# Kernel optimization log

Measured on AMD Instinct MI355X. Metric: run time of the kernel, lower is better.

## Reference

```python
import jax, jax.numpy as jnp
import numpy as np

N, NFEAT, NHID, NCLASS = 8192, 128, 128, 40


def _init(key, shape, fan_in):
    return jax.random.normal(key, shape, jnp.float32) / np.sqrt(fan_in).astype(np.float32)


def setup_inputs() -> dict:
    ks = jax.random.split(jax.random.key(0), 8)
    return {
        "x": jax.random.normal(ks[0], (N, NFEAT), jnp.float32),
        # dense normalized adjacency: row-stochastic-ish positive matrix
        "adj": jax.random.uniform(ks[1], (N, N), jnp.float32) * (2.0 / N),
        "W_emb": _init(ks[2], (NFEAT, NHID), NFEAT),
        "b_emb": jnp.zeros((NHID,), jnp.float32),
        "W_gc1": _init(ks[3], (NHID, NHID), NHID),
        "b_gc1": jnp.zeros((NHID,), jnp.float32),
        "W_e": _init(ks[4], (2 * NHID, NHID), 2 * NHID),
        "b_e": jnp.zeros((NHID,), jnp.float32),
        "W_gc2": _init(ks[5], (NHID, NCLASS), NHID),
        "b_gc2": jnp.zeros((NCLASS,), jnp.float32),
        "fully_connected_graph": 1,  # unused by forward (passed but never read)
    }


def reference(x, adj, W_emb, b_emb, W_gc1, b_gc1, W_e, b_e, W_gc2, b_gc2,
              fully_connected_graph):
    nhid = W_emb.shape[1]
    # x = self.emb(x)
    h = x @ W_emb + b_emb  # [N, nhid]

    # Edge branch. Original materializes edge_feat[i*N+j] = concat(h[i], h[j])
    # ([N*N, 2*nhid]) then GraphConvolution_edge: support = edge_feat @ W_e,
    # reshaped [N, N, nhid], aggregated x_e[i] = sum_j adj[i,j] * support[i,j] + b_e.
    # Algebraically identical fused form (same math, no O(N^2*nhid) tensor):
    #   support[i,j] = h[i] @ W_e[:nhid] + h[j] @ W_e[nhid:]
    #   x_e[i] = deg[i] * (h[i] @ W_e_src) + (adj @ (h @ W_e_dst))[i] + b_e
    s_src = h @ W_e[:nhid]   # [N, nhid]
    s_dst = h @ W_e[nhid:]   # [N, nhid]
    deg = adj.sum(axis=1, keepdims=True)  # [N, 1] row sums
    x_e = deg * s_src + adj @ s_dst + b_e  # [N, nhid]

    # Node branch: gc1 -> relu -> dropout(eval: identity) -> gc2 -> log_softmax
    h1 = jax.nn.relu(adj @ (h @ W_gc1) + b_gc1)       # [N, nhid]
    logits = adj @ (h1 @ W_gc2) + b_gc2               # [N, nclass]
    out = jax.nn.log_softmax(logits, axis=1)
    return out, x_e
```

## Files before the change

### kernel.cpp

```cpp
#include <hip/hip_runtime.h>

#define DI __device__ __forceinline__

using f32x4  = __attribute__((ext_vector_type(4))) float;
using bf16x8 = __attribute__((ext_vector_type(8))) __bf16;
using u16x4  = __attribute__((ext_vector_type(4))) unsigned short;
using u32x4  = __attribute__((ext_vector_type(4))) unsigned int;

constexpr int NNODE = 8192;

DI unsigned short f2bf(float f) {
    unsigned int u = __builtin_bit_cast(unsigned int, f);
    u += 0x7fffu + ((u >> 16) & 1u);
    return (unsigned short)(u >> 16);
}
DI float bf2f(unsigned short s) {
    return __builtin_bit_cast(float, (unsigned int)s << 16);
}

DI int swz256(int r, int cb) { return r * 256 + (cb ^ ((r & 15) << 4)); }
DI int swz128(int r, int cb) { return r * 128 + (cb ^ ((r & 7) << 4)); }

__global__ void prep_w(const float* __restrict__ W_emb, const float* __restrict__ W_e,
                       const float* __restrict__ W_gc1, const float* __restrict__ W_gc2,
                       unsigned short* __restrict__ WembT_hi, unsigned short* __restrict__ WembT_lo,
                       unsigned short* __restrict__ WcatT_hi, unsigned short* __restrict__ WcatT_lo,
                       unsigned short* __restrict__ Wg2T_hi, unsigned short* __restrict__ Wg2T_lo)
{
    int gid = blockIdx.x * 256 + threadIdx.x;
    if (gid >= 576 * 128) return;
    int k = gid & 127, n = gid >> 7;
    float v;
    unsigned short *dh, *dl;
    if (n < 128) {
        v = W_emb[k * 128 + n];
        dh = WembT_hi + n * 128 + k; dl = WembT_lo + n * 128 + k;
    } else if (n < 512) {
        int m = n - 128;
        if (m < 128)      v = W_e[k * 128 + m];
        else if (m < 256) v = W_e[(k + 128) * 128 + (m - 128)];
        else              v = W_gc1[k * 128 + (m - 256)];
        dh = WcatT_hi + m * 128 + k; dl = WcatT_lo + m * 128 + k;
    } else {
        int c = n - 512;
        v = (c < 40) ? W_gc2[k * 40 + c] : 0.f;
        dh = Wg2T_hi + c * 128 + k; dl = Wg2T_lo + c * 128 + k;
    }
    unsigned short hi = f2bf(v);
    *dh = hi;
    *dl = f2bf(v - bf2f(hi));
}

template<int NCHUNK, int AKIND, int OUTKIND>
__global__ __launch_bounds__(256) void small_gemm(
    const float* __restrict__ Af32,
    const unsigned short* __restrict__ A_hi, const unsigned short* __restrict__ A_lo,
    const unsigned short* __restrict__ Bt_hi, const unsigned short* __restrict__ Bt_lo,
    const float* __restrict__ bias,
    unsigned short* __restrict__ out_hi, unsigned short* __restrict__ out_lo,
    float* __restrict__ out_s,
    unsigned short* __restrict__ out_t)
{
    __shared__ unsigned short Ah[64 * 128], Al[64 * 128];
    __shared__ unsigned short Bh[NCHUNK * 128], Bl[NCHUNK * 128];
    char* Ahc = (char*)Ah; char* Alc = (char*)Al;
    char* Bhc = (char*)Bh; char* Blc = (char*)Bl;

    const int tid = threadIdx.x;
    const int r0 = blockIdx.x * 64;
    const int n0 = blockIdx.y * NCHUNK;

    if constexpr (AKIND == 0) {
        #pragma unroll
        for (int p = 0; p < 8; ++p) {
            int idx = tid + 256 * p, r = idx >> 5, c4 = idx & 31;
            f32x4 v = *(const f32x4*)(Af32 + (size_t)(r0 + r) * 128 + c4 * 4);
            u16x4 ph, pl;
            #pragma unroll
            for (int j = 0; j < 4; ++j) {
                unsigned short hi = f2bf(v[j]);
                ph[j] = hi; pl[j] = f2bf(v[j] - bf2f(hi));
            }
            *(u16x4*)(Ahc + swz256(r, c4 * 8)) = ph;
            *(u16x4*)(Alc + swz256(r, c4 * 8)) = pl;
        }
    } else {
        #pragma unroll
        for (int p = 0; p < 4; ++p) {
            int idx = tid + 256 * p, r = idx >> 4, c = idx & 15;
            u32x4 vh = *(const u32x4*)(A_hi + (size_t)(r0 + r) * 128 + c * 8);
            u32x4 vl = *(const u32x4*)(A_lo + (size_t)(r0 + r) * 128 + c * 8);
            *(u32x4*)(Ahc + swz256(r, c * 16)) = vh;
            *(u32x4*)(Alc + swz256(r, c * 16)) = vl;
        }
    }
    #pragma unroll
    for (int p = 0; p < NCHUNK / 16; ++p) {
        int idx = tid + 256 * p, r = idx >> 4, c = idx & 15;
        u32x4 vh = *(const u32x4*)(Bt_hi + (size_t)(n0 + r) * 128 + c * 8);
        u32x4 vl = *(const u32x4*)(Bt_lo + (size_t)(n0 + r) * 128 + c * 8);
        *(u32x4*)(Bhc + swz256(r, c * 16)) = vh;
        *(u32x4*)(Blc + swz256(r, c * 16)) = vl;
    }
    __syncthreads();

    const int lane = tid & 63, wid = tid >> 6;
    const int lrow = lane & 15, lkb = (lane >> 4) * 16;
    constexpr int FN = NCHUNK / 16;
    f32x4 acc[FN];
    #pragma unroll
    for (int i = 0; i < FN; ++i) acc[i] = f32x4{0.f, 0.f, 0.f, 0.f};

    const int arow = wid * 16 + lrow;
    #pragma unroll
    for (int kk = 0; kk < 4; ++kk) {
        bf16x8 ah = *(const bf16x8*)(Ahc + swz256(arow, kk * 64 + lkb));
        bf16x8 al = *(const bf16x8*)(Alc + swz256(arow, kk * 64 + lkb));
        #pragma unroll
        for (int nf = 0; nf < FN; ++nf) {
            bf16x8 bh = *(const bf16x8*)(Bhc + swz256(nf * 16 + lrow, kk * 64 + lkb));
            bf16x8 bl = *(const bf16x8*)(Blc + swz256(nf * 16 + lrow, kk * 64 + lkb));
            acc[nf] = __builtin_amdgcn_mfma_f32_16x16x32_bf16(ah, bh, acc[nf], 0, 0, 0);
            acc[nf] = __builtin_amdgcn_mfma_f32_16x16x32_bf16(ah, bl, acc[nf], 0, 0, 0);
            acc[nf] = __builtin_amdgcn_mfma_f32_16x16x32_bf16(al, bh, acc[nf], 0, 0, 0);
        }
    }

    const int rowb = r0 + wid * 16 + ((lane >> 4) << 2);
    #pragma unroll
    for (int nf = 0; nf < FN; ++nf) {
        const int col = n0 + nf * 16 + lrow;
        if constexpr (OUTKIND == 0) {
            float bv = bias[col];
            #pragma unroll
            for (int j = 0; j < 4; ++j) {
                float v = acc[nf][j] + bv;
                unsigned short hi = f2bf(v);
                out_hi[(size_t)(rowb + j) * 128 + col] = hi;
                out_lo[(size_t)(rowb + j) * 128 + col] = f2bf(v - bf2f(hi));
            }
        } else if constexpr (OUTKIND == 1) {
            if (col < 128) {
                #pragma unroll
                for (int j = 0; j < 4; ++j)
                    out_s[(size_t)(rowb + j) * 128 + col] = acc[nf][j];
            } else {
                u16x4 pk = { f2bf(acc[nf][0]), f2bf(acc[nf][1]), f2bf(acc[nf][2]), f2bf(acc[nf][3]) };
                *(u16x4*)(out_t + (size_t)(col - 128) * NNODE + rowb) = pk;
            }
        } else {
            u16x4 pk = { f2bf(acc[nf][0]), f2bf(acc[nf][1]), f2bf(acc[nf][2]), f2bf(acc[nf][3]) };
            *(u16x4*)(out_t + (size_t)col * NNODE + rowb) = pk;
        }
    }
}

template<int NCOLS, int KSPLIT, bool DEG, bool REV>
__global__ __launch_bounds__(512, 4) void adj_gemm(
    const float* __restrict__ adj,
    const unsigned short* __restrict__ Bt,
    float* __restrict__ Tpart,
    float* __restrict__ deg)
{
    __shared__ unsigned short A_lds[2][64 * 64];
    __shared__ unsigned short B_lds[2][NCOLS * 64];

    const int tid = threadIdx.x;
    const int r0 = blockIdx.x * 64;
    const int ks = blockIdx.y;
    constexpr int KLEN = NNODE / KSPLIT;
    constexpr int NT = KLEN / 64;
    const int kbase = ks * KLEN;

    constexpr int NB = NCOLS / 64;
    f32x4 areg[2];
    u32x4 breg[NB];
    float dsum0 = 0.f, dsum1 = 0.f;
    const int ar0 = tid >> 4, ac4 = tid & 15;

    const int lane = tid & 63, wid = tid >> 6;
    constexpr int FM = (NCOLS == 256) ? 2 : 1;
    constexpr int FN = (NCOLS == 256) ? 4 : 2;
    const int wr = (NCOLS == 256) ? (wid >> 2) : (wid >> 1);
    const int wc = (NCOLS == 256) ? (wid & 3) : (wid & 1);
    const int row_w = wr * FM * 16, col_w = wc * FN * 16;
    const int lrow = lane & 15, lkb = (lane >> 4) * 16;

    f32x4 acc[FM][FN];
    #pragma unroll
    for (int fm = 0; fm < FM; ++fm)
        #pragma unroll
        for (int fn = 0; fn < FN; ++fn) acc[fm][fn] = f32x4{0.f, 0.f, 0.f, 0.f};

    auto order = [&](int tt) { return REV ? (NT - 1 - tt) : tt; };

    auto loadG = [&](int t) {
        const int kt = kbase + t * 64;
        #pragma unroll
        for (int p = 0; p < 2; ++p) {
            areg[p] = *(const f32x4*)(adj + (size_t)(r0 + ar0 + 32 * p) * NNODE + kt + ac4 * 4);
            if (DEG) {
                float s = areg[p][0] + areg[p][1] + areg[p][2] + areg[p][3];
                if (p == 0) dsum0 += s; else dsum1 += s;
            }
        }
        #pragma unroll
        for (int p = 0; p < NB; ++p) {
            const int idx = tid + 512 * p, n = idx >> 3, c = idx & 7;
            breg[p] = *(const u32x4*)(Bt + (size_t)n * NNODE + kt + c * 8);
        }
    };
    auto storeL = [&](int buf) {
        char* Ac = (char*)(A_lds[buf]);
        char* Bc = (char*)(B_lds[buf]);
        #pragma unroll
        for (int p = 0; p < 2; ++p) {
            u16x4 pk = { f2bf(areg[p][0]), f2bf(areg[p][1]), f2bf(areg[p][2]), f2bf(areg[p][3]) };
            *(u16x4*)(Ac + swz128(ar0 + 32 * p, ac4 * 8)) = pk;
        }
        #pragma unroll
        for (int p = 0; p < NB; ++p) {
            const int idx = tid + 512 * p, n = idx >> 3, c = idx & 7;
            *(u32x4*)(Bc + swz128(n, c * 16)) = breg[p];
        }
    };

    loadG(order(0));
    storeL(0);
    for (int tt = 0; tt < NT; ++tt) {
        if (tt + 1 < NT) loadG(order(tt + 1));
        __syncthreads();
        const char* Ac = (const char*)(A_lds[tt & 1]);
        const char* Bc = (const char*)(B_lds[tt & 1]);
        #pragma unroll
        for (int kk = 0; kk < 2; ++kk) {
            bf16x8 a[FM], b[FN];
            #pragma unroll
            for (int fm = 0; fm < FM; ++fm)
                a[fm] = *(const bf16x8*)(Ac + swz128(row_w + fm * 16 + lrow, kk * 64 + lkb));
            #pragma unroll
            for (int fn = 0; fn < FN; ++fn)
                b[fn] = *(const bf16x8*)(Bc + swz128(col_w + fn * 16 + lrow, kk * 64 + lkb));
            #pragma unroll
            for (int fm = 0; fm < FM; ++fm)
                #pragma unroll
                for (int fn = 0; fn < FN; ++fn)
                    acc[fm][fn] = __builtin_amdgcn_mfma_f32_16x16x32_bf16(a[fm], b[fn], acc[fm][fn], 0, 0, 0);
        }
        if (tt + 1 < NT) storeL((tt + 1) & 1);
    }

    float* outp = Tpart + (size_t)ks * NNODE * NCOLS;
    #pragma unroll
    for (int fm = 0; fm < FM; ++fm) {
        const int grow0 = r0 + row_w + fm * 16 + ((lane >> 4) << 2);
        #pragma unroll
        for (int fn = 0; fn < FN; ++fn) {
            const int gcol = col_w + fn * 16 + lrow;
            #pragma unroll
            for (int j = 0; j < 4; ++j)
                outp[(size_t)(grow0 + j) * NCOLS + gcol] = acc[fm][fn][j];
        }
    }

    if (DEG) {
        __syncthreads();
        float* sc = (float*)(&A_lds[0][0]);
        sc[tid] = dsum0;
        sc[512 + tid] = dsum1;
        __syncthreads();
        if (tid < 64) {
            const int base = (tid < 32) ? tid * 16 : (512 + (tid - 32) * 16);
            float s = 0.f;
            #pragma unroll
            for (int i = 0; i < 16; ++i) s += sc[base + i];
            atomicAdd(deg + r0 + tid, s);
        }
    }
}

template<int KSPLIT>
__global__ void post1(const float* __restrict__ tA,
                      const float* __restrict__ s_src,
                      const float* __restrict__ deg,
                      const float* __restrict__ b_e,
                      const float* __restrict__ b_gc1,
                      float* __restrict__ x_e_out,
                      unsigned short* __restrict__ h1_hi, unsigned short* __restrict__ h1_lo)
{
    int gid = blockIdx.x * 256 + threadIdx.x;
    int i = gid >> 7, c = gid & 127;
    const size_t o = (size_t)i * 256;
    float t_sdst = 0.f, t_g1 = 0.f;
    #pragma unroll
    for (int p = 0; p < KSPLIT; ++p) {
        const size_t op = (size_t)p * NNODE * 256 + o;
        t_sdst += tA[op + c];
        t_g1   += tA[op + 128 + c];
    }
    x_e_out[gid] = deg[i] * s_src[gid] + t_sdst + b_e[c];
    float h1 = t_g1 + b_gc1[c];
    h1 = h1 > 0.f ? h1 : 0.f;
    unsigned short hi = f2bf(h1);
    h1_hi[gid] = hi;
    h1_lo[gid] = f2bf(h1 - bf2f(hi));
}

template<int KSPLIT>
__global__ void logsm(const float* __restrict__ tB,
                      const float* __restrict__ b_gc2,
                      float* __restrict__ out)
{
    const int wid = threadIdx.x >> 6, lane = threadIdx.x & 63;
    const int row = blockIdx.x * 4 + wid;
    float v = -1e30f;
    if (lane < 40) {
        float s = b_gc2[lane];
        #pragma unroll
        for (int p = 0; p < KSPLIT; ++p)
            s += tB[(size_t)p * NNODE * 64 + (size_t)row * 64 + lane];
        v = s;
    }
    float m = v;
    #pragma unroll
    for (int off = 32; off; off >>= 1) m = fmaxf(m, __shfl_xor(m, off, 64));
    float e = (lane < 40) ? expf(v - m) : 0.f;
    float s = e;
    #pragma unroll
    for (int off = 32; off; off >>= 1) s += __shfl_xor(s, off, 64);
    if (lane < 40) out[(size_t)row * 40 + lane] = v - m - logf(s);
}

extern "C" void kernel_launch(void* const* d_in, const int* in_sizes, int n_in,
                              void* d_out, int out_size, void* d_ws, size_t ws_size,
                              hipStream_t stream)
{
    const float* x     = (const float*)d_in[0];
    const float* adj   = (const float*)d_in[1];
    const float* W_emb = (const float*)d_in[2];
    const float* b_emb = (const float*)d_in[3];
    const float* W_gc1 = (const float*)d_in[4];
    const float* b_gc1 = (const float*)d_in[5];
    const float* W_e   = (const float*)d_in[6];
    const float* b_e   = (const float*)d_in[7];
    const float* W_gc2 = (const float*)d_in[8];
    const float* b_gc2 = (const float*)d_in[9];

    constexpr int KSA = 4;
    constexpr int KSB = 8;

    char* p = (char*)d_ws;
    auto take = [&](size_t bytes) { char* q = p; p += (bytes + 255) & ~(size_t)255; return q; };

    unsigned short* WembT_hi = (unsigned short*)take(128 * 128 * 2);
    unsigned short* WembT_lo = (unsigned short*)take(128 * 128 * 2);
    unsigned short* WcatT_hi = (unsigned short*)take(384 * 128 * 2);
    unsigned short* WcatT_lo = (unsigned short*)take(384 * 128 * 2);
    unsigned short* Wg2T_hi  = (unsigned short*)take(64 * 128 * 2);
    unsigned short* Wg2T_lo  = (unsigned short*)take(64 * 128 * 2);
    unsigned short* h_hi     = (unsigned short*)take((size_t)NNODE * 128 * 2);
    unsigned short* h_lo     = (unsigned short*)take((size_t)NNODE * 128 * 2);
    float*          s_src    = (float*)take((size_t)NNODE * 128 * 4);
    unsigned short* B_A      = (unsigned short*)take((size_t)256 * NNODE * 2);
    float*          tA       = (float*)take((size_t)KSA * NNODE * 256 * 4);
    float*          deg      = (float*)take((size_t)NNODE * 4);
    unsigned short* B_B   = (unsigned short*)s_src;
    float*          tB    = tA;
    unsigned short* h1_hi = h_hi;
    unsigned short* h1_lo = h_lo;

    float* out_ls = (float*)d_out;
    float* x_e    = (float*)d_out + (size_t)NNODE * 40;

    hipMemsetAsync(deg, 0, NNODE * sizeof(float), stream);
    prep_w<<<288, 256, 0, stream>>>(W_emb, W_e, W_gc1, W_gc2,
                                    WembT_hi, WembT_lo, WcatT_hi, WcatT_lo, Wg2T_hi, Wg2T_lo);
    small_gemm<128, 0, 0><<<dim3(128, 1), 256, 0, stream>>>(
        x, nullptr, nullptr, WembT_hi, WembT_lo, b_emb, h_hi, h_lo, nullptr, nullptr);
    small_gemm<128, 1, 1><<<dim3(128, 3), 256, 0, stream>>>(
        nullptr, h_hi, h_lo, WcatT_hi, WcatT_lo, nullptr, nullptr, nullptr, s_src, B_A);
    adj_gemm<256, KSA, true, false><<<dim3(128, KSA), 512, 0, stream>>>(adj, B_A, tA, deg);
    post1<KSA><<<4096, 256, 0, stream>>>(tA, s_src, deg, b_e, b_gc1, x_e, h1_hi, h1_lo);
    small_gemm<64, 1, 2><<<dim3(128, 1), 256, 0, stream>>>(
        nullptr, h1_hi, h1_lo, Wg2T_hi, Wg2T_lo, nullptr, nullptr, nullptr, nullptr, B_B);
    adj_gemm<64, KSB, false, true><<<dim3(128, KSB), 512, 0, stream>>>(adj, B_B, tB, nullptr);
    logsm<KSB><<<2048, 256, 0, stream>>>(tB, b_gc2, out_ls);
}
```

Baseline: 164.5 us.

## Cache bf16 copy of adjacency in first pass and reuse it in second pass

The first adjacency GEMM now writes the bf16-converted adj tiles to a workspace buffer. The second adjacency GEMM reads that half-size bf16 copy instead of the fp32 matrix and skips the conversion. The K-split factors for both GEMMs are halved and the occupancy hint in launch bounds is dropped. This adds a large 128MB write in the first pass and needs extra workspace, so total DRAM traffic is roughly unchanged unless the copy stays in the last-level cache.

```diff
diff --git a/kernel.cpp b/kernel.cpp
--- a/kernel.cpp
+++ b/kernel.cpp
@@ -155,9 +155,11 @@
     }
 }
 
-template<int NCOLS, int KSPLIT, bool DEG, bool REV>
-__global__ __launch_bounds__(512, 4) void adj_gemm(
-    const float* __restrict__ adj,
+template<int NCOLS, int KSPLIT, bool DEG, bool REV, int AMODE>
+__global__ __launch_bounds__(512) void adj_gemm(
+    const float* __restrict__ adjf,
+    const unsigned short* __restrict__ adjb,
+    unsigned short* __restrict__ adjb_out,
     const unsigned short* __restrict__ Bt,
     float* __restrict__ Tpart,
     float* __restrict__ deg)
@@ -174,9 +176,11 @@
 
     constexpr int NB = NCOLS / 64;
     f32x4 areg[2];
+    u32x4 aregb;
     u32x4 breg[NB];
     float dsum0 = 0.f, dsum1 = 0.f;
     const int ar0 = tid >> 4, ac4 = tid & 15;
+    const int br0 = tid >> 3, bc = tid & 7;
 
     const int lane = tid & 63, wid = tid >> 6;
     constexpr int FM = (NCOLS == 256) ? 2 : 1;
@@ -196,13 +200,17 @@
 
     auto loadG = [&](int t) {
         const int kt = kbase + t * 64;
-        #pragma unroll
-        for (int p = 0; p < 2; ++p) {
-            areg[p] = *(const f32x4*)(adj + (size_t)(r0 + ar0 + 32 * p) * NNODE + kt + ac4 * 4);
-            if (DEG) {
-                float s = areg[p][0] + areg[p][1] + areg[p][2] + areg[p][3];
-                if (p == 0) dsum0 += s; else dsum1 += s;
+        if constexpr (AMODE == 0) {
+            #pragma unroll
+            for (int p = 0; p < 2; ++p) {
+                areg[p] = *(const f32x4*)(adjf + (size_t)(r0 + ar0 + 32 * p) * NNODE + kt + ac4 * 4);
+                if (DEG) {
+                    float s = areg[p][0] + areg[p][1] + areg[p][2] + areg[p][3];
+                    if (p == 0) dsum0 += s; else dsum1 += s;
+                }
             }
+        } else {
+            aregb = *(const u32x4*)(adjb + (size_t)(r0 + br0) * NNODE + kt + bc * 8);
         }
         #pragma unroll
         for (int p = 0; p < NB; ++p) {
@@ -210,13 +218,19 @@
             breg[p] = *(const u32x4*)(Bt + (size_t)n * NNODE + kt + c * 8);
         }
     };
-    auto storeL = [&](int buf) {
+    auto storeL = [&](int buf, int t) {
+        const int kt = kbase + t * 64;
         char* Ac = (char*)(A_lds[buf]);
         char* Bc = (char*)(B_lds[buf]);
-        #pragma unroll
-        for (int p = 0; p < 2; ++p) {
-            u16x4 pk = { f2bf(areg[p][0]), f2bf(areg[p][1]), f2bf(areg[p][2]), f2bf(areg[p][3]) };
-            *(u16x4*)(Ac + swz128(ar0 + 32 * p, ac4 * 8)) = pk;
+        if constexpr (AMODE == 0) {
+            #pragma unroll
+            for (int p = 0; p < 2; ++p) {
+                u16x4 pk = { f2bf(areg[p][0]), f2bf(areg[p][1]), f2bf(areg[p][2]), f2bf(areg[p][3]) };
+                *(u16x4*)(Ac + swz128(ar0 + 32 * p, ac4 * 8)) = pk;
+                *(u16x4*)(adjb_out + (size_t)(r0 + ar0 + 32 * p) * NNODE + kt + ac4 * 4) = pk;
+            }
+        } else {
+            *(u32x4*)(Ac + swz128(br0, bc * 16)) = aregb;
         }
         #pragma unroll
         for (int p = 0; p < NB; ++p) {
@@ -226,7 +240,7 @@
     };
 
     loadG(order(0));
-    storeL(0);
+    storeL(0, order(0));
     for (int tt = 0; tt < NT; ++tt) {
         if (tt + 1 < NT) loadG(order(tt + 1));
         __syncthreads();
@@ -247,7 +261,7 @@
                 for (int fn = 0; fn < FN; ++fn)
                     acc[fm][fn] = __builtin_amdgcn_mfma_f32_16x16x32_bf16(a[fm], b[fn], acc[fm][fn], 0, 0, 0);
         }
-        if (tt + 1 < NT) storeL((tt + 1) & 1);
+        if (tt + 1 < NT) storeL((tt + 1) & 1, order(tt + 1));
     }
 
     float* outp = Tpart + (size_t)ks * NNODE * NCOLS;
@@ -346,8 +360,8 @@
     const float* W_gc2 = (const float*)d_in[8];
     const float* b_gc2 = (const float*)d_in[9];
 
-    constexpr int KSA = 4;
-    constexpr int KSB = 8;
+    constexpr int KSA = 2;
+    constexpr int KSB = 4;
 
     char* p = (char*)d_ws;
     auto take = [&](size_t bytes) { char* q = p; p += (bytes + 255) & ~(size_t)255; return q; };
@@ -364,6 +378,7 @@
     unsigned short* B_A      = (unsigned short*)take((size_t)256 * NNODE * 2);
     float*          tA       = (float*)take((size_t)KSA * NNODE * 256 * 4);
     float*          deg      = (float*)take((size_t)NNODE * 4);
+    unsigned short* adjb     = (unsigned short*)take((size_t)NNODE * NNODE * 2);
     unsigned short* B_B   = (unsigned short*)s_src;
     float*          tB    = tA;
     unsigned short* h1_hi = h_hi;
@@ -379,10 +394,12 @@
         x, nullptr, nullptr, WembT_hi, WembT_lo, b_emb, h_hi, h_lo, nullptr, nullptr);
     small_gemm<128, 1, 1><<<dim3(128, 3), 256, 0, stream>>>(
         nullptr, h_hi, h_lo, WcatT_hi, WcatT_lo, nullptr, nullptr, nullptr, s_src, B_A);
-    adj_gemm<256, KSA, true, false><<<dim3(128, KSA), 512, 0, stream>>>(adj, B_A, tA, deg);
+    adj_gemm<256, KSA, true, false, 0><<<dim3(128, KSA), 512, 0, stream>>>(
+        adj, nullptr, adjb, B_A, tA, deg);
     post1<KSA><<<4096, 256, 0, stream>>>(tA, s_src, deg, b_e, b_gc1, x_e, h1_hi, h1_lo);
     small_gemm<64, 1, 2><<<dim3(128, 1), 256, 0, stream>>>(
         nullptr, h1_hi, h1_lo, Wg2T_hi, Wg2T_lo, nullptr, nullptr, nullptr, nullptr, B_B);
-    adj_gemm<64, KSB, false, true><<<dim3(128, KSB), 512, 0, stream>>>(adj, B_B, tB, nullptr);
+    adj_gemm<64, KSB, false, true, 1><<<dim3(128, KSB), 512, 0, stream>>>(
+        nullptr, adjb, nullptr, B_B, tB, nullptr);
     logsm<KSB><<<2048, 256, 0, stream>>>(tB, b_gc2, out_ls);
 }
```

Measured after the change: 180.5 us. 1.1x slower.

## Fuse small GEMMs and post-processing, drop deg atomics, reduce split-K factors

Applied to the files above, without the earlier changes.

Merges the embedding GEMM and the concatenated-weight GEMM into one kernel that keeps h in LDS. It also fuses the post1 elementwise step with the h1@W_gc2 GEMM and replaces the atomic degree accumulation and its memset with per-split partial sums. Split-K drops from 4/8 to 2 for both adjacency GEMMs, and the occupancy hint is removed from adj_gemm. This cuts launches and intermediate round trips to global memory, at the cost of fewer blocks (only 128-256) for the adjacency GEMMs and less parallelism in the fused kernels.

```diff
diff --git a/kernel.cpp b/kernel.cpp
--- a/kernel.cpp
+++ b/kernel.cpp
@@ -51,116 +51,112 @@
     *dl = f2bf(v - bf2f(hi));
 }
 
-template<int NCHUNK, int AKIND, int OUTKIND>
-__global__ __launch_bounds__(256) void small_gemm(
-    const float* __restrict__ Af32,
-    const unsigned short* __restrict__ A_hi, const unsigned short* __restrict__ A_lo,
-    const unsigned short* __restrict__ Bt_hi, const unsigned short* __restrict__ Bt_lo,
-    const float* __restrict__ bias,
-    unsigned short* __restrict__ out_hi, unsigned short* __restrict__ out_lo,
+__global__ __launch_bounds__(512) void gemm_hs(
+    const float* __restrict__ x,
+    const unsigned short* __restrict__ WembT_hi, const unsigned short* __restrict__ WembT_lo,
+    const unsigned short* __restrict__ WcatT_hi, const unsigned short* __restrict__ WcatT_lo,
+    const float* __restrict__ b_emb,
     float* __restrict__ out_s,
     unsigned short* __restrict__ out_t)
 {
-    __shared__ unsigned short Ah[64 * 128], Al[64 * 128];
-    __shared__ unsigned short Bh[NCHUNK * 128], Bl[NCHUNK * 128];
-    char* Ahc = (char*)Ah; char* Alc = (char*)Al;
-    char* Bhc = (char*)Bh; char* Blc = (char*)Bl;
+    __shared__ unsigned short Hh[64 * 128], Hl[64 * 128];
+    char* Hhc = (char*)Hh; char* Hlc = (char*)Hl;
 
     const int tid = threadIdx.x;
     const int r0 = blockIdx.x * 64;
-    const int n0 = blockIdx.y * NCHUNK;
-
-    if constexpr (AKIND == 0) {
-        #pragma unroll
-        for (int p = 0; p < 8; ++p) {
-            int idx = tid + 256 * p, r = idx >> 5, c4 = idx & 31;
-            f32x4 v = *(const f32x4*)(Af32 + (size_t)(r0 + r) * 128 + c4 * 4);
-            u16x4 ph, pl;
-            #pragma unroll
-            for (int j = 0; j < 4; ++j) {
-                unsigned short hi = f2bf(v[j]);
-                ph[j] = hi; pl[j] = f2bf(v[j] - bf2f(hi));
-            }
-            *(u16x4*)(Ahc + swz256(r, c4 * 8)) = ph;
-            *(u16x4*)(Alc + swz256(r, c4 * 8)) = pl;
-        }
-    } else {
-        #pragma unroll
-        for (int p = 0; p < 4; ++p) {
-            int idx = tid + 256 * p, r = idx >> 4, c = idx & 15;
-            u32x4 vh = *(const u32x4*)(A_hi + (size_t)(r0 + r) * 128 + c * 8);
-            u32x4 vl = *(const u32x4*)(A_lo + (size_t)(r0 + r) * 128 + c * 8);
-            *(u32x4*)(Ahc + swz256(r, c * 16)) = vh;
-            *(u32x4*)(Alc + swz256(r, c * 16)) = vl;
-        }
-    }
-    #pragma unroll
-    for (int p = 0; p < NCHUNK / 16; ++p) {
-        int idx = tid + 256 * p, r = idx >> 4, c = idx & 15;
-        u32x4 vh = *(const u32x4*)(Bt_hi + (size_t)(n0 + r) * 128 + c * 8);
-        u32x4 vl = *(const u32x4*)(Bt_lo + (size_t)(n0 + r) * 128 + c * 8);
-        *(u32x4*)(Bhc + swz256(r, c * 16)) = vh;
-        *(u32x4*)(Blc + swz256(r, c * 16)) = vl;
+    const int lane = tid & 63, wid = tid >> 6;
+    const int lrow = lane & 15, lk8 = (lane >> 4) * 8, lkb = (lane >> 4) * 16;
+    const int wrg = wid & 3;
+    const int wcg = wid >> 2;
+
+    #pragma unroll
+    for (int p = 0; p < 4; ++p) {
+        int idx = tid + 512 * p, r = idx >> 5, c4 = idx & 31;
+        f32x4 v = *(const f32x4*)(x + (size_t)(r0 + r) * 128 + c4 * 4);
+        u16x4 ph, pl;
+        #pragma unroll
+        for (int j = 0; j < 4; ++j) {
+            unsigned short hi = f2bf(v[j]);
+            ph[j] = hi; pl[j] = f2bf(v[j] - bf2f(hi));
+        }
+        *(u16x4*)(Hhc + swz256(r, c4 * 8)) = ph;
+        *(u16x4*)(Hlc + swz256(r, c4 * 8)) = pl;
     }
     __syncthreads();
 
-    const int lane = tid & 63, wid = tid >> 6;
-    const int lrow = lane & 15, lkb = (lane >> 4) * 16;
-    constexpr int FN = NCHUNK / 16;
-    f32x4 acc[FN];
-    #pragma unroll
-    for (int i = 0; i < FN; ++i) acc[i] = f32x4{0.f, 0.f, 0.f, 0.f};
-
-    const int arow = wid * 16 + lrow;
+    f32x4 acc[4];
+    #pragma unroll
+    for (int i = 0; i < 4; ++i) acc[i] = f32x4{0.f, 0.f, 0.f, 0.f};
+    const int arow = wrg * 16 + lrow;
     #pragma unroll
     for (int kk = 0; kk < 4; ++kk) {
-        bf16x8 ah = *(const bf16x8*)(Ahc + swz256(arow, kk * 64 + lkb));
-        bf16x8 al = *(const bf16x8*)(Alc + swz256(arow, kk * 64 + lkb));
-        #pragma unroll
-        for (int nf = 0; nf < FN; ++nf) {
-            bf16x8 bh = *(const bf16x8*)(Bhc + swz256(nf * 16 + lrow, kk * 64 + lkb));
-            bf16x8 bl = *(const bf16x8*)(Blc + swz256(nf * 16 + lrow, kk * 64 + lkb));
+        bf16x8 ah = *(const bf16x8*)(Hhc + swz256(arow, kk * 64 + lkb));
+        bf16x8 al = *(const bf16x8*)(Hlc + swz256(arow, kk * 64 + lkb));
+        #pragma unroll
+        for (int nf = 0; nf < 4; ++nf) {
+            const int n = wcg * 64 + nf * 16 + lrow;
+            bf16x8 bh = *(const bf16x8*)(WembT_hi + (size_t)n * 128 + kk * 32 + lk8);
+            bf16x8 bl = *(const bf16x8*)(WembT_lo + (size_t)n * 128 + kk * 32 + lk8);
             acc[nf] = __builtin_amdgcn_mfma_f32_16x16x32_bf16(ah, bh, acc[nf], 0, 0, 0);
             acc[nf] = __builtin_amdgcn_mfma_f32_16x16x32_bf16(ah, bl, acc[nf], 0, 0, 0);
             acc[nf] = __builtin_amdgcn_mfma_f32_16x16x32_bf16(al, bh, acc[nf], 0, 0, 0);
         }
     }
-
-    const int rowb = r0 + wid * 16 + ((lane >> 4) << 2);
-    #pragma unroll
-    for (int nf = 0; nf < FN; ++nf) {
-        const int col = n0 + nf * 16 + lrow;
-        if constexpr (OUTKIND == 0) {
-            float bv = bias[col];
-            #pragma unroll
-            for (int j = 0; j < 4; ++j) {
-                float v = acc[nf][j] + bv;
-                unsigned short hi = f2bf(v);
-                out_hi[(size_t)(rowb + j) * 128 + col] = hi;
-                out_lo[(size_t)(rowb + j) * 128 + col] = f2bf(v - bf2f(hi));
-            }
-        } else if constexpr (OUTKIND == 1) {
-            if (col < 128) {
-                #pragma unroll
-                for (int j = 0; j < 4; ++j)
-                    out_s[(size_t)(rowb + j) * 128 + col] = acc[nf][j];
-            } else {
-                u16x4 pk = { f2bf(acc[nf][0]), f2bf(acc[nf][1]), f2bf(acc[nf][2]), f2bf(acc[nf][3]) };
-                *(u16x4*)(out_t + (size_t)(col - 128) * NNODE + rowb) = pk;
-            }
+    __syncthreads();
+
+    #pragma unroll
+    for (int nf = 0; nf < 4; ++nf) {
+        const int col = wcg * 64 + nf * 16 + lrow;
+        const float bv = b_emb[col];
+        #pragma unroll
+        for (int j = 0; j < 4; ++j) {
+            const int row = wrg * 16 + ((lane >> 4) << 2) + j;
+            float v = acc[nf][j] + bv;
+            unsigned short hi = f2bf(v);
+            *(unsigned short*)(Hhc + swz256(row, col * 2)) = hi;
+            *(unsigned short*)(Hlc + swz256(row, col * 2)) = f2bf(v - bf2f(hi));
+        }
+    }
+    __syncthreads();
+
+    f32x4 acc2[12];
+    #pragma unroll
+    for (int i = 0; i < 12; ++i) acc2[i] = f32x4{0.f, 0.f, 0.f, 0.f};
+    #pragma unroll
+    for (int kk = 0; kk < 4; ++kk) {
+        bf16x8 ah = *(const bf16x8*)(Hhc + swz256(arow, kk * 64 + lkb));
+        bf16x8 al = *(const bf16x8*)(Hlc + swz256(arow, kk * 64 + lkb));
+        #pragma unroll
+        for (int nf = 0; nf < 12; ++nf) {
+            const int n = wcg * 192 + nf * 16 + lrow;
+            bf16x8 bh = *(const bf16x8*)(WcatT_hi + (size_t)n * 128 + kk * 32 + lk8);
+            bf16x8 bl = *(const bf16x8*)(WcatT_lo + (size_t)n * 128 + kk * 32 + lk8);
+            acc2[nf] = __builtin_amdgcn_mfma_f32_16x16x32_bf16(ah, bh, acc2[nf], 0, 0, 0);
+            acc2[nf] = __builtin_amdgcn_mfma_f32_16x16x32_bf16(ah, bl, acc2[nf], 0, 0, 0);
+            acc2[nf] = __builtin_amdgcn_mfma_f32_16x16x32_bf16(al, bh, acc2[nf], 0, 0, 0);
+        }
+    }
+    const int rowb = r0 + wrg * 16 + ((lane >> 4) << 2);
+    #pragma unroll
+    for (int nf = 0; nf < 12; ++nf) {
+        const int col = wcg * 192 + nf * 16 + lrow;
+        if (wcg == 0 && nf < 8) {
+            #pragma unroll
+            for (int j = 0; j < 4; ++j)
+                out_s[(size_t)(rowb + j) * 128 + col] = acc2[nf][j];
         } else {
-            u16x4 pk = { f2bf(acc[nf][0]), f2bf(acc[nf][1]), f2bf(acc[nf][2]), f2bf(acc[nf][3]) };
-            *(u16x4*)(out_t + (size_t)col * NNODE + rowb) = pk;
+            u16x4 pk = { f2bf(acc2[nf][0]), f2bf(acc2[nf][1]), f2bf(acc2[nf][2]), f2bf(acc2[nf][3]) };
+            *(u16x4*)(out_t + (size_t)(col - 128) * NNODE + rowb) = pk;
         }
     }
 }
 
 template<int NCOLS, int KSPLIT, bool DEG, bool REV>
-__global__ __launch_bounds__(512, 4) void adj_gemm(
+__global__ __launch_bounds__(512) void adj_gemm(
     const float* __restrict__ adj,
     const unsigned short* __restrict__ Bt,
     float* __restrict__ Tpart,
-    float* __restrict__ deg)
+    float* __restrict__ degp)
 {
     __shared__ unsigned short A_lds[2][64 * 64];
     __shared__ unsigned short B_lds[2][NCOLS * 64];
@@ -274,36 +270,90 @@
             float s = 0.f;
             #pragma unroll
             for (int i = 0; i < 16; ++i) s += sc[base + i];
-            atomicAdd(deg + r0 + tid, s);
-        }
-    }
-}
-
-template<int KSPLIT>
-__global__ void post1(const float* __restrict__ tA,
-                      const float* __restrict__ s_src,
-                      const float* __restrict__ deg,
-                      const float* __restrict__ b_e,
-                      const float* __restrict__ b_gc1,
-                      float* __restrict__ x_e_out,
-                      unsigned short* __restrict__ h1_hi, unsigned short* __restrict__ h1_lo)
-{
-    int gid = blockIdx.x * 256 + threadIdx.x;
-    int i = gid >> 7, c = gid & 127;
-    const size_t o = (size_t)i * 256;
-    float t_sdst = 0.f, t_g1 = 0.f;
-    #pragma unroll
-    for (int p = 0; p < KSPLIT; ++p) {
-        const size_t op = (size_t)p * NNODE * 256 + o;
-        t_sdst += tA[op + c];
-        t_g1   += tA[op + 128 + c];
-    }
-    x_e_out[gid] = deg[i] * s_src[gid] + t_sdst + b_e[c];
-    float h1 = t_g1 + b_gc1[c];
-    h1 = h1 > 0.f ? h1 : 0.f;
-    unsigned short hi = f2bf(h1);
-    h1_hi[gid] = hi;
-    h1_lo[gid] = f2bf(h1 - bf2f(hi));
+            degp[(size_t)ks * NNODE + r0 + tid] = s;
+        }
+    }
+}
+
+template<int KSA>
+__global__ __launch_bounds__(256) void post1g2(
+    const float* __restrict__ tA,
+    const float* __restrict__ s_src,
+    const float* __restrict__ degp,
+    const float* __restrict__ b_e,
+    const float* __restrict__ b_gc1,
+    const unsigned short* __restrict__ Wg2T_hi, const unsigned short* __restrict__ Wg2T_lo,
+    float* __restrict__ x_e_out,
+    unsigned short* __restrict__ out_t)
+{
+    __shared__ unsigned short Hh[64 * 128], Hl[64 * 128];
+    char* Hhc = (char*)Hh; char* Hlc = (char*)Hl;
+
+    const int tid = threadIdx.x;
+    const int r0 = blockIdx.x * 64;
+
+    #pragma unroll
+    for (int p = 0; p < 8; ++p) {
+        int idx = tid + 256 * p, r = idx >> 5, c4 = idx & 31;
+        const int gi = r0 + r;
+        float dv = 0.f;
+        #pragma unroll
+        for (int q = 0; q < KSA; ++q) dv += degp[(size_t)q * NNODE + gi];
+        f32x4 sdst = f32x4{0.f, 0.f, 0.f, 0.f}, g1 = f32x4{0.f, 0.f, 0.f, 0.f};
+        #pragma unroll
+        for (int q = 0; q < KSA; ++q) {
+            const float* tp = tA + (size_t)q * NNODE * 256 + (size_t)gi * 256;
+            f32x4 a = *(const f32x4*)(tp + c4 * 4);
+            f32x4 b = *(const f32x4*)(tp + 128 + c4 * 4);
+            #pragma unroll
+            for (int j = 0; j < 4; ++j) { sdst[j] += a[j]; g1[j] += b[j]; }
+        }
+        f32x4 ss = *(const f32x4*)(s_src + (size_t)gi * 128 + c4 * 4);
+        f32x4 be = *(const f32x4*)(b_e + c4 * 4);
+        f32x4 bg = *(const f32x4*)(b_gc1 + c4 * 4);
+        f32x4 xe;
+        u16x4 ph, pl;
+        #pragma unroll
+        for (int j = 0; j < 4; ++j) {
+            xe[j] = dv * ss[j] + sdst[j] + be[j];
+            float h1 = g1[j] + bg[j];
+            h1 = h1 > 0.f ? h1 : 0.f;
+            unsigned short hi = f2bf(h1);
+            ph[j] = hi; pl[j] = f2bf(h1 - bf2f(hi));
+        }
+        *(f32x4*)(x_e_out + (size_t)gi * 128 + c4 * 4) = xe;
+        *(u16x4*)(Hhc + swz256(r, c4 * 8)) = ph;
+        *(u16x4*)(Hlc + swz256(r, c4 * 8)) = pl;
+    }
+    __syncthreads();
+
+    const int lane = tid & 63, wid = tid >> 6;
+    const int lrow = lane & 15, lk8 = (lane >> 4) * 8, lkb = (lane >> 4) * 16;
+    f32x4 acc[4];
+    #pragma unroll
+    for (int i = 0; i < 4; ++i) acc[i] = f32x4{0.f, 0.f, 0.f, 0.f};
+    const int arow = wid * 16 + lrow;
+    #pragma unroll
+    for (int kk = 0; kk < 4; ++kk) {
+        bf16x8 ah = *(const bf16x8*)(Hhc + swz256(arow, kk * 64 + lkb));
+        bf16x8 al = *(const bf16x8*)(Hlc + swz256(arow, kk * 64 + lkb));
+        #pragma unroll
+        for (int nf = 0; nf < 4; ++nf) {
+            const int n = nf * 16 + lrow;
+            bf16x8 bh = *(const bf16x8*)(Wg2T_hi + (size_t)n * 128 + kk * 32 + lk8);
+            bf16x8 bl = *(const bf16x8*)(Wg2T_lo + (size_t)n * 128 + kk * 32 + lk8);
+            acc[nf] = __builtin_amdgcn_mfma_f32_16x16x32_bf16(ah, bh, acc[nf], 0, 0, 0);
+            acc[nf] = __builtin_amdgcn_mfma_f32_16x16x32_bf16(ah, bl, acc[nf], 0, 0, 0);
+            acc[nf] = __builtin_amdgcn_mfma_f32_16x16x32_bf16(al, bh, acc[nf], 0, 0, 0);
+        }
+    }
+    const int rowb = r0 + wid * 16 + ((lane >> 4) << 2);
+    #pragma unroll
+    for (int nf = 0; nf < 4; ++nf) {
+        const int col = nf * 16 + lrow;
+        u16x4 pk = { f2bf(acc[nf][0]), f2bf(acc[nf][1]), f2bf(acc[nf][2]), f2bf(acc[nf][3]) };
+        *(u16x4*)(out_t + (size_t)col * NNODE + rowb) = pk;
+    }
 }
 
 template<int KSPLIT>
@@ -346,8 +396,8 @@
     const float* W_gc2 = (const float*)d_in[8];
     const float* b_gc2 = (const float*)d_in[9];
 
-    constexpr int KSA = 4;
-    constexpr int KSB = 8;
+    constexpr int KSA = 2;
+    constexpr int KSB = 2;
 
     char* p = (char*)d_ws;
     auto take = [&](size_t bytes) { char* q = p; p += (bytes + 255) & ~(size_t)255; return q; };
@@ -358,31 +408,23 @@
     unsigned short* WcatT_lo = (unsigned short*)take(384 * 128 * 2);
     unsigned short* Wg2T_hi  = (unsigned short*)take(64 * 128 * 2);
     unsigned short* Wg2T_lo  = (unsigned short*)take(64 * 128 * 2);
-    unsigned short* h_hi     = (unsigned short*)take((size_t)NNODE * 128 * 2);
-    unsigned short* h_lo     = (unsigned short*)take((size_t)NNODE * 128 * 2);
     float*          s_src    = (float*)take((size_t)NNODE * 128 * 4);
     unsigned short* B_A      = (unsigned short*)take((size_t)256 * NNODE * 2);
+    unsigned short* B_B      = (unsigned short*)take((size_t)64 * NNODE * 2);
     float*          tA       = (float*)take((size_t)KSA * NNODE * 256 * 4);
-    float*          deg      = (float*)take((size_t)NNODE * 4);
-    unsigned short* B_B   = (unsigned short*)s_src;
-    float*          tB    = tA;
-    unsigned short* h1_hi = h_hi;
-    unsigned short* h1_lo = h_lo;
+    float*          tB       = (float*)take((size_t)KSB * NNODE * 64 * 4);
+    float*          degp     = (float*)take((size_t)KSA * NNODE * 4);
 
     float* out_ls = (float*)d_out;
     float* x_e    = (float*)d_out + (size_t)NNODE * 40;
 
-    hipMemsetAsync(deg, 0, NNODE * sizeof(float), stream);
     prep_w<<<288, 256, 0, stream>>>(W_emb, W_e, W_gc1, W_gc2,
                                     WembT_hi, WembT_lo, WcatT_hi, WcatT_lo, Wg2T_hi, Wg2T_lo);
-    small_gemm<128, 0, 0><<<dim3(128, 1), 256, 0, stream>>>(
-        x, nullptr, nullptr, WembT_hi, WembT_lo, b_emb, h_hi, h_lo, nullptr, nullptr);
-    small_gemm<128, 1, 1><<<dim3(128, 3), 256, 0, stream>>>(
-        nullptr, h_hi, h_lo, WcatT_hi, WcatT_lo, nullptr, nullptr, nullptr, s_src, B_A);
-    adj_gemm<256, KSA, true, false><<<dim3(128, KSA), 512, 0, stream>>>(adj, B_A, tA, deg);
-    post1<KSA><<<4096, 256, 0, stream>>>(tA, s_src, deg, b_e, b_gc1, x_e, h1_hi, h1_lo);
-    small_gemm<64, 1, 2><<<dim3(128, 1), 256, 0, stream>>>(
-        nullptr, h1_hi, h1_lo, Wg2T_hi, Wg2T_lo, nullptr, nullptr, nullptr, nullptr, B_B);
+    gemm_hs<<<128, 512, 0, stream>>>(x, WembT_hi, WembT_lo, WcatT_hi, WcatT_lo, b_emb,
+                                     s_src, B_A);
+    adj_gemm<256, KSA, true, false><<<dim3(128, KSA), 512, 0, stream>>>(adj, B_A, tA, degp);
+    post1g2<KSA><<<128, 256, 0, stream>>>(tA, s_src, degp, b_e, b_gc1,
+                                          Wg2T_hi, Wg2T_lo, x_e, B_B);
     adj_gemm<64, KSB, false, true><<<dim3(128, KSB), 512, 0, stream>>>(adj, B_B, tB, nullptr);
     logsm<KSB><<<2048, 256, 0, stream>>>(tB, b_gc2, out_ls);
 }
```

After: 163.7 us. About the same (-0.5%).
